# Performance work log

Measured on AMD Instinct MI355X. Metric: run time of the kernel, lower is better.

The kernel has to match this reference:

```python
import jax, jax.numpy as jnp
import numpy as np

B, T, V, D = 4, 2048, 1024, 512


def setup_inputs() -> dict:
    key = jax.random.key(0)
    ks = jax.random.split(key, 6)
    x = jax.random.normal(ks[0], (B, T, V), dtype=jnp.float32)
    decay_logit = jax.random.uniform(ks[1], (), dtype=jnp.float32)
    scale = jnp.ones((), dtype=jnp.float32)
    std = 0.02
    # Linear weights stored as [in, out] so projection is x @ W
    Wq = std * jax.random.normal(ks[2], (V, D), dtype=jnp.float32)
    Wk = std * jax.random.normal(ks[3], (V, D), dtype=jnp.float32)
    Wv = std * jax.random.normal(ks[4], (V, D), dtype=jnp.float32)
    Wo = std * jax.random.normal(ks[5], (D, V), dtype=jnp.float32)
    return {"x": x, "decay_logit": decay_logit, "scale": scale,
            "Wq": Wq, "Wk": Wk, "Wv": Wv, "Wo": Wo}


def reference(x, decay_logit, scale, Wq, Wk, Wv, Wo):
    dtype = x.dtype
    xf = x.astype(jnp.float32)
    q = (xf @ Wq).astype(dtype)  # [B,T,D]
    k = (xf @ Wk).astype(dtype)
    v = (xf @ Wv).astype(dtype)
    scores = jnp.einsum('btd,bsd->bts', q, k)  # [B,T,T]
    decay = jax.nn.sigmoid(decay_logit)
    pos = jnp.arange(T)
    diff = pos[None, :] - pos[:, None]  # diff[i,j] = j - i
    expo = jnp.maximum(diff.astype(jnp.float32) - 1.0, 0.0)
    weights = (decay ** expo) * (diff > 0)  # [T,T]
    scores = scores * weights.astype(dtype)[None, :, :]
    retrieved = jnp.einsum('bts,bsd->btd', scores, v)  # [B,T,D]
    out = (retrieved.astype(jnp.float32) @ Wo).astype(dtype) * scale
    return out
```

## Files before the change

### kernel.cpp

```cpp
#include <hip/hip_runtime.h>
#include <stdint.h>


using bf16u = unsigned short;
using short8 = __attribute__((ext_vector_type(8))) short;
using f32x4  = __attribute__((ext_vector_type(4))) float;

__device__ __forceinline__ unsigned short f2bf(float f) {
  unsigned int u = __float_as_uint(f);
  u += 0x7fffu + ((u >> 16) & 1u);
  return (unsigned short)(u >> 16);
}

__device__ __forceinline__ void gload16(const void* g, void* l) {
  __builtin_amdgcn_global_load_lds(
      (const __attribute__((address_space(1))) void*)g,
      (__attribute__((address_space(3))) void*)l, 16, 0, 0);
}

#define BM 128
#define BN 128
#define BK 32

template<int MODE>
__global__ __launch_bounds__(256)
void gemm_bt(const bf16u* __restrict__ A, const bf16u* __restrict__ Bt,
             void* __restrict__ Cout,
             int K, int ldA, int ldB, int ldC,
             long sA, long sB, long sC,
             int nbx, const float* __restrict__ scal)
{
  __shared__ bf16u Al[2][BM * BK];
  __shared__ bf16u Bl[2][BN * BK];
  const int z = blockIdx.z;
  A  += (long)z * sA;
  Bt += (long)z * sB;

  const int nwg  = gridDim.x;
  const int orig = blockIdx.x;
  const int q8 = nwg >> 3, r8 = nwg & 7;
  const int xcd = orig & 7, lid = orig >> 3;
  const int wgid = (xcd < r8 ? xcd * (q8 + 1)
                             : r8 * (q8 + 1) + (xcd - r8) * q8) + lid;
  const int by = wgid / nbx, bx = wgid - by * nbx;
  const int bm = by * BM;
  const int bn = (MODE == 1) ? (by + bx) * BN : bx * BN;
  const int kofsB = (MODE == 3) ? bm : 0;

  const int tid  = threadIdx.x;
  const int wid  = tid >> 6;
  const int lane = tid & 63;
  const int wr = (wid >> 1) * 64;
  const int wc = (wid & 1) * 64;

  f32x4 acc[4][4] = {};

  const int base0 = wid * 1024;
  const int lin0  = base0 + lane * 16;
  const int r0row = lin0 >> 6;
  const int r1row = r0row + 64;
  const int c16   = (lin0 >> 4) & 3;
  const int rcol  = (c16 ^ ((r0row >> 1) & 3)) << 3;

  const int nt = K / BK;

  auto stage = [&](int buf, int kk) {
    gload16(A  + (long)(bm + r0row) * ldA + kk + rcol, (char*)&Al[buf][0] + base0);
    gload16(A  + (long)(bm + r1row) * ldA + kk + rcol, (char*)&Al[buf][0] + base0 + 4096);
    gload16(Bt + (long)(bn + r0row) * ldB + kofsB + kk + rcol, (char*)&Bl[buf][0] + base0);
    gload16(Bt + (long)(bn + r1row) * ldB + kofsB + kk + rcol, (char*)&Bl[buf][0] + base0 + 4096);
  };

  stage(0, 0);
  __syncthreads();

  const int fr = lane & 15;
  const int kc = lane >> 4;
  int cur = 0;
  for (int t = 0; t < nt; ++t) {
    if (t + 1 < nt) stage(cur ^ 1, (t + 1) * BK);
    short8 af[4], bfr[4];
#pragma unroll
    for (int m = 0; m < 4; ++m) {
      int row = wr + m * 16 + fr;
      af[m] = *(const short8*)&Al[cur][row * BK + ((kc ^ ((row >> 1) & 3)) << 3)];
    }
#pragma unroll
    for (int n = 0; n < 4; ++n) {
      int row = wc + n * 16 + fr;
      bfr[n] = *(const short8*)&Bl[cur][row * BK + ((kc ^ ((row >> 1) & 3)) << 3)];
    }
#pragma unroll
    for (int m = 0; m < 4; ++m)
#pragma unroll
      for (int n = 0; n < 4; ++n)
        acc[m][n] = __builtin_amdgcn_mfma_f32_16x16x32_bf16(af[m], bfr[n], acc[m][n], 0, 0, 0);
    __syncthreads();
    cur ^= 1;
  }

  const int cc = lane & 15;
  const int cr = (lane >> 4) * 4;
  float mul = 1.0f, l2d = 0.0f;
  if (MODE == 1) {
    float dlv = scal[0];
    float decay = 1.0f / (1.0f + __expf(-dlv));
    l2d = __log2f(decay);
  } else if (MODE == 2) {
    mul = scal[0];
  }

#pragma unroll
  for (int m = 0; m < 4; ++m) {
#pragma unroll
    for (int n = 0; n < 4; ++n) {
#pragma unroll
      for (int j = 0; j < 4; ++j) {
        int row = bm + wr + m * 16 + cr + j;
        int col = bn + wc + n * 16 + cc;
        float val = acc[m][n][j];
        if (MODE == 1) {
          int diff = col - row;
          float w = (diff > 0 && col < 2048)
                        ? exp2f((float)(diff - 1) * l2d) : 0.0f;
          int lc = bx * 128 + (wc + n * 16 + cc);
          ((bf16u*)Cout)[(long)z * sC + (long)row * ldC + lc] = f2bf(val * w);
        } else if (MODE == 2) {
          ((float*)Cout)[(long)z * sC + (long)row * ldC + col] = val * mul;
        } else {
          ((bf16u*)Cout)[(long)z * sC + (long)row * ldC + col] = f2bf(val);
        }
      }
    }
  }
}

__global__ void cvt4(const float4* __restrict__ in, ushort4* __restrict__ out, int n4) {
  int i = blockIdx.x * 256 + threadIdx.x;
  if (i < n4) {
    float4 v = in[i];
    ushort4 o;
    o.x = f2bf(v.x); o.y = f2bf(v.y); o.z = f2bf(v.z); o.w = f2bf(v.w);
    out[i] = o;
  }
}

__global__ void tconvAll(const float* __restrict__ Wq, const float* __restrict__ Wk,
                         const float* __restrict__ Wv, const float* __restrict__ Wo,
                         bf16u* __restrict__ WqT, bf16u* __restrict__ WkT,
                         bf16u* __restrict__ WvT, bf16u* __restrict__ WoT,
                         int V, int D) {
  __shared__ float t[32][33];
  const int zz = blockIdx.z;
  const float* in; bf16u* out; int R, C;
  if (zz == 0)      { in = Wq; out = WqT; R = V; C = D; }
  else if (zz == 1) { in = Wk; out = WkT; R = V; C = D; }
  else if (zz == 2) { in = Wv; out = WvT; R = V; C = D; }
  else              { in = Wo; out = WoT; R = D; C = V; }
  int c0 = blockIdx.x * 32, r0 = blockIdx.y * 32;
  if (c0 >= C || r0 >= R) return;
  int tx = threadIdx.x, ty = threadIdx.y;
#pragma unroll
  for (int i = 0; i < 4; ++i)
    t[ty + 8 * i][tx] = in[(long)(r0 + ty + 8 * i) * C + c0 + tx];
  __syncthreads();
#pragma unroll
  for (int i = 0; i < 4; ++i)
    out[(long)(c0 + ty + 8 * i) * R + r0 + tx] = f2bf(t[tx][ty + 8 * i]);
}

__global__ void tr16(const bf16u* __restrict__ in, bf16u* __restrict__ out,
                     int R, int C, int ldIn, long sIn, long sOut) {
  __shared__ bf16u t[32][33];
  in  += (long)blockIdx.z * sIn;
  out += (long)blockIdx.z * sOut;
  int c0 = blockIdx.x * 32, r0 = blockIdx.y * 32;
  int tx = threadIdx.x, ty = threadIdx.y;
#pragma unroll
  for (int i = 0; i < 4; ++i)
    t[ty + 8 * i][tx] = in[(long)(r0 + ty + 8 * i) * ldIn + c0 + tx];
  __syncthreads();
#pragma unroll
  for (int i = 0; i < 4; ++i)
    out[(long)(c0 + ty + 8 * i) * R + r0 + tx] = t[tx][ty + 8 * i];
}

extern "C" void kernel_launch(void* const* d_in, const int* in_sizes, int n_in,
                              void* d_out, int out_size, void* d_ws, size_t ws_size,
                              hipStream_t stream) {
  const float* x  = (const float*)d_in[0];
  const float* dl = (const float*)d_in[1];
  const float* sc = (const float*)d_in[2];
  const float* Wq = (const float*)d_in[3];
  const float* Wk = (const float*)d_in[4];
  const float* Wv = (const float*)d_in[5];
  const float* Wo = (const float*)d_in[6];

  const int B = 4, T = 2048, V = 1024, D = 512;
  const long MT = (long)B * T;
  const int QKV = 3 * D;
  const int BAND = 256;

  char* p = (char*)d_ws;
  auto alloc = [&](size_t bytes) { char* r = p; p += bytes; return r; };
  bf16u* x16 = (bf16u*)alloc((size_t)MT * V * 2);
  bf16u* WqT = (bf16u*)alloc((size_t)D * V * 2);
  bf16u* WkT = (bf16u*)alloc((size_t)D * V * 2);
  bf16u* WvT = (bf16u*)alloc((size_t)D * V * 2);
  bf16u* WoT = (bf16u*)alloc((size_t)V * D * 2);
  bf16u* qkv = (bf16u*)alloc((size_t)MT * QKV * 2);
  bf16u* vT  = (bf16u*)alloc((size_t)MT * D * 2 + 4096);
  bf16u* Sb  = (bf16u*)alloc((size_t)B * T * BAND * 2);
  bf16u* R   = (bf16u*)alloc((size_t)MT * D * 2);

  int n4 = (int)(MT * V / 4);
  cvt4<<<(n4 + 255) / 256, 256, 0, stream>>>((const float4*)x, (ushort4*)x16, n4);

  tconvAll<<<dim3(32, 32, 4), dim3(32, 8), 0, stream>>>(
      Wq, Wk, Wv, Wo, WqT, WkT, WvT, WoT, V, D);

  gemm_bt<0><<<dim3(64 * 12, 1, 1), 256, 0, stream>>>(
      x16, WqT, qkv, V, V, V, QKV, 0, 0, 0, 12, nullptr);

  tr16<<<dim3(D / 32, T / 32, B), dim3(32, 8), 0, stream>>>(
      qkv + 2 * D, vT, T, D, QKV, (long)T * QKV, (long)D * T);

  gemm_bt<1><<<dim3(16 * 2, 1, B), 256, 0, stream>>>(
      qkv, qkv + D, Sb, D, QKV, QKV, BAND,
      (long)T * QKV, (long)T * QKV, (long)T * BAND, 2, dl);

  gemm_bt<3><<<dim3(16 * 4, 1, B), 256, 0, stream>>>(
      Sb, vT, R, BAND, BAND, T, D,
      (long)T * BAND, (long)1 << 20, (long)T * D, 4, nullptr);

  gemm_bt<2><<<dim3(64 * 8, 1, 1), 256, 0, stream>>>(
      R, WoT, d_out, D, D, D, V, 0, 0, 0, 8, sc);
}
```

Before: 96.31 us.

## Triple-buffer GEMM pipeline with vmcnt waits and template tile shapes

Converts the GEMM main loop from double-buffered with two full syncthreads per step to a three-stage LDS ring that prefetches two tiles ahead. It waits on vmcnt counters and a single raw barrier instead. Tile sizes become template parameters: smaller 128x64 or 64x128 tiles raise the block count for each GEMM, and launch bounds request 4 waves per SIMD. The intent is to hide global-load latency and improve occupancy and CU fill, at the cost of more LDS per block and less reuse per tile.

```diff
diff --git a/kernel.cpp b/kernel.cpp
--- a/kernel.cpp
+++ b/kernel.cpp
@@ -18,20 +18,29 @@
       (__attribute__((address_space(3))) void*)l, 16, 0, 0);
 }
 
-#define BM 128
-#define BN 128
+template<int N> __device__ __forceinline__ void waitvm() {
+  if constexpr (N == 0)      asm volatile("s_waitcnt vmcnt(0)" ::: "memory");
+  else if constexpr (N == 3) asm volatile("s_waitcnt vmcnt(3)" ::: "memory");
+  else                       asm volatile("s_waitcnt vmcnt(4)" ::: "memory");
+}
+
 #define BK 32
 
-template<int MODE>
-__global__ __launch_bounds__(256)
+template<int MODE, int TBM, int TBN>
+__global__ __launch_bounds__(256, 4)
 void gemm_bt(const bf16u* __restrict__ A, const bf16u* __restrict__ Bt,
              void* __restrict__ Cout,
              int K, int ldA, int ldB, int ldC,
              long sA, long sB, long sC,
              int nbx, const float* __restrict__ scal)
 {
-  __shared__ bf16u Al[2][BM * BK];
-  __shared__ bf16u Bl[2][BN * BK];
+  constexpr int WR = TBM / 2, WC = TBN / 2;
+  constexpr int MF = WR / 16, NF = WC / 16;
+  constexpr int RA = TBM / 64, RB = TBN / 64;
+  constexpr int L  = RA + RB;
+
+  __shared__ bf16u Al[3][TBM * BK];
+  __shared__ bf16u Bl[3][TBN * BK];
   const int z = blockIdx.z;
   A  += (long)z * sA;
   Bt += (long)z * sB;
@@ -43,60 +52,69 @@
   const int wgid = (xcd < r8 ? xcd * (q8 + 1)
                              : r8 * (q8 + 1) + (xcd - r8) * q8) + lid;
   const int by = wgid / nbx, bx = wgid - by * nbx;
-  const int bm = by * BM;
-  const int bn = (MODE == 1) ? (by + bx) * BN : bx * BN;
-  const int kofsB = (MODE == 3) ? bm : 0;
+  const int bm = by * TBM;
+  const int rb128 = bm >> 7;
+  const int bn = (MODE == 1) ? (rb128 + bx) * TBN : bx * TBN;
+  const int kofsB = (MODE == 3) ? (bm & ~127) : 0;
 
   const int tid  = threadIdx.x;
   const int wid  = tid >> 6;
   const int lane = tid & 63;
-  const int wr = (wid >> 1) * 64;
-  const int wc = (wid & 1) * 64;
-
-  f32x4 acc[4][4] = {};
+  const int wr = (wid >> 1) * WR;
+  const int wc = (wid & 1) * WC;
+
+  f32x4 acc[MF][NF] = {};
 
   const int base0 = wid * 1024;
   const int lin0  = base0 + lane * 16;
   const int r0row = lin0 >> 6;
-  const int r1row = r0row + 64;
   const int c16   = (lin0 >> 4) & 3;
   const int rcol  = (c16 ^ ((r0row >> 1) & 3)) << 3;
 
   const int nt = K / BK;
 
   auto stage = [&](int buf, int kk) {
-    gload16(A  + (long)(bm + r0row) * ldA + kk + rcol, (char*)&Al[buf][0] + base0);
-    gload16(A  + (long)(bm + r1row) * ldA + kk + rcol, (char*)&Al[buf][0] + base0 + 4096);
-    gload16(Bt + (long)(bn + r0row) * ldB + kofsB + kk + rcol, (char*)&Bl[buf][0] + base0);
-    gload16(Bt + (long)(bn + r1row) * ldB + kofsB + kk + rcol, (char*)&Bl[buf][0] + base0 + 4096);
+#pragma unroll
+    for (int r = 0; r < RA; ++r)
+      gload16(A + (long)(bm + r * 64 + r0row) * ldA + kk + rcol,
+              (char*)&Al[buf][0] + r * 4096 + base0);
+#pragma unroll
+    for (int r = 0; r < RB; ++r)
+      gload16(Bt + (long)(bn + r * 64 + r0row) * ldB + kofsB + kk + rcol,
+              (char*)&Bl[buf][0] + r * 4096 + base0);
   };
 
   stage(0, 0);
-  __syncthreads();
+  if (nt > 1) stage(1, BK);
 
   const int fr = lane & 15;
   const int kc = lane >> 4;
   int cur = 0;
   for (int t = 0; t < nt; ++t) {
-    if (t + 1 < nt) stage(cur ^ 1, (t + 1) * BK);
-    short8 af[4], bfr[4];
-#pragma unroll
-    for (int m = 0; m < 4; ++m) {
+    if (t + 1 < nt) waitvm<L>(); else waitvm<0>();
+    __builtin_amdgcn_s_barrier();
+    __builtin_amdgcn_sched_barrier(0);
+    if (t + 2 < nt) {
+      int nx = cur + 2; if (nx >= 3) nx -= 3;
+      stage(nx, (t + 2) * BK);
+    }
+    short8 af[MF], bfr[NF];
+#pragma unroll
+    for (int m = 0; m < MF; ++m) {
       int row = wr + m * 16 + fr;
       af[m] = *(const short8*)&Al[cur][row * BK + ((kc ^ ((row >> 1) & 3)) << 3)];
     }
 #pragma unroll
-    for (int n = 0; n < 4; ++n) {
+    for (int n = 0; n < NF; ++n) {
       int row = wc + n * 16 + fr;
       bfr[n] = *(const short8*)&Bl[cur][row * BK + ((kc ^ ((row >> 1) & 3)) << 3)];
     }
 #pragma unroll
-    for (int m = 0; m < 4; ++m)
-#pragma unroll
-      for (int n = 0; n < 4; ++n)
+    for (int m = 0; m < MF; ++m)
+#pragma unroll
+      for (int n = 0; n < NF; ++n)
         acc[m][n] = __builtin_amdgcn_mfma_f32_16x16x32_bf16(af[m], bfr[n], acc[m][n], 0, 0, 0);
-    __syncthreads();
-    cur ^= 1;
+    ++cur; if (cur == 3) cur = 0;
   }
 
   const int cc = lane & 15;
@@ -111,9 +129,9 @@
   }
 
 #pragma unroll
-  for (int m = 0; m < 4; ++m) {
-#pragma unroll
-    for (int n = 0; n < 4; ++n) {
+  for (int m = 0; m < MF; ++m) {
+#pragma unroll
+    for (int n = 0; n < NF; ++n) {
 #pragma unroll
       for (int j = 0; j < 4; ++j) {
         int row = bm + wr + m * 16 + cr + j;
@@ -219,20 +237,20 @@
   tconvAll<<<dim3(32, 32, 4), dim3(32, 8), 0, stream>>>(
       Wq, Wk, Wv, Wo, WqT, WkT, WvT, WoT, V, D);
 
-  gemm_bt<0><<<dim3(64 * 12, 1, 1), 256, 0, stream>>>(
-      x16, WqT, qkv, V, V, V, QKV, 0, 0, 0, 12, nullptr);
+  gemm_bt<0, 128, 64><<<dim3(64 * 24, 1, 1), 256, 0, stream>>>(
+      x16, WqT, qkv, V, V, V, QKV, 0, 0, 0, 24, nullptr);
 
   tr16<<<dim3(D / 32, T / 32, B), dim3(32, 8), 0, stream>>>(
       qkv + 2 * D, vT, T, D, QKV, (long)T * QKV, (long)D * T);
 
-  gemm_bt<1><<<dim3(16 * 2, 1, B), 256, 0, stream>>>(
+  gemm_bt<1, 64, 128><<<dim3(32 * 2, 1, B), 256, 0, stream>>>(
       qkv, qkv + D, Sb, D, QKV, QKV, BAND,
       (long)T * QKV, (long)T * QKV, (long)T * BAND, 2, dl);
 
-  gemm_bt<3><<<dim3(16 * 4, 1, B), 256, 0, stream>>>(
+  gemm_bt<3, 64, 128><<<dim3(32 * 4, 1, B), 256, 0, stream>>>(
       Sb, vT, R, BAND, BAND, T, D,
       (long)T * BAND, (long)1 << 20, (long)T * D, 4, nullptr);
 
-  gemm_bt<2><<<dim3(64 * 8, 1, 1), 256, 0, stream>>>(
-      R, WoT, d_out, D, D, D, V, 0, 0, 0, 8, sc);
-}
+  gemm_bt<2, 128, 64><<<dim3(64 * 16, 1, 1), 256, 0, stream>>>(
+      R, WoT, d_out, D, D, D, V, 0, 0, 0, 16, sc);
+}
```

After: 105.5 us. 9.5% more time.
